# Performance work log

Hardware: AMD Instinct MI355X
Metric: run time of the kernel (lower is better)

The kernel has to match this reference:

```python
import jax, jax.numpy as jnp
import numpy as np

N_NODES = 100000


def gcn_conv(x, src, dst, W, b, n):
    # PyG GCNConv: x' = D^-1/2 (A + I) D^-1/2 (x W) + b
    h = x @ W  # [N, out] transform first (cheaper when out < in)
    loop = jnp.arange(n, dtype=src.dtype)
    s = jnp.concatenate([src, loop])
    d = jnp.concatenate([dst, loop])
    deg = jax.ops.segment_sum(jnp.ones_like(s, dtype=h.dtype), d, num_segments=n)
    dinv = jnp.where(deg > 0, jax.lax.rsqrt(deg), 0.0)
    norm = dinv[s] * dinv[d]  # [E+N]
    msg = h[s] * norm[:, None]  # [E+N, out]
    agg = jax.ops.segment_sum(msg, d, num_segments=n)
    return agg + b


def setup_inputs() -> dict:
    key = jax.random.key(0)
    ks = jax.random.split(key, 12)
    n, E, labels = N_NODES, 1600000, 128
    edges = jax.random.randint(ks[0], (2, E), 0, n, dtype=jnp.int64)
    features = jax.random.normal(ks[1], (n, labels), dtype=jnp.float32)

    def kaiming(k, fan_in, shape):
        return jax.random.normal(k, shape, dtype=jnp.float32) * np.sqrt(2.0 / fan_in)

    return {
        "edges": edges,
        "features": features,
        "W1": kaiming(ks[2], labels, (labels, 64)),
        "b1": jnp.zeros((64,), jnp.float32),
        "W2": kaiming(ks[3], 64, (64, 32)),
        "b2": jnp.zeros((32,), jnp.float32),
        "W3": kaiming(ks[4], 32, (32, 16)),
        "b3": jnp.zeros((16,), jnp.float32),
        "Wfc": kaiming(ks[5], 112, (112, 16)),
        "bfc": jnp.zeros((16,), jnp.float32),
    }


def reference(edges, features, W1, b1, W2, b2, W3, b3, Wfc, bfc):
    n = features.shape[0]
    src, dst = edges[0], edges[1]
    # eval mode: dropout is identity
    f1 = jax.nn.relu(gcn_conv(features, src, dst, W1, b1, n))  # [N, 64]
    f2 = jax.nn.relu(gcn_conv(f1, src, dst, W2, b2, n))        # [N, 32]
    f3 = jax.nn.relu(gcn_conv(f2, src, dst, W3, b3, n))        # [N, 16]
    cat = jnp.concatenate([f1, f2, f3], axis=1)                 # [N, 112]
    return jax.nn.relu(cat @ Wfc + bfc)                         # [N, 16]
```

## Files before the change

### kernel.cpp

```cpp
#include <hip/hip_runtime.h>

typedef unsigned short u16;
typedef float f32x4 __attribute__((ext_vector_type(4)));
typedef short bf16x8 __attribute__((ext_vector_type(8)));

constexpr int SH = 9;
constexpr int NB = 1 << SH;
constexpr int TILE = 4096;

__device__ inline float bf2f(u16 u) {
  union { unsigned int i; float f; } c;
  c.i = ((unsigned int)u) << 16;
  return c.f;
}
__device__ inline u16 f2bf(float f) {
  union { float f; unsigned int i; } c;
  c.f = f;
  unsigned int r = c.i + 0x7fff + ((c.i >> 16) & 1);
  return (u16)(r >> 16);
}

union V8 {
  bf16x8 v;
  short s[8];
  u16 u[8];
};


__global__ void __launch_bounds__(256) k_hist(const int* __restrict__ dst,
                                              int* __restrict__ ghist, int E,
                                              int nblk, int nbk) {
  __shared__ int lcnt[NB];
  int t = threadIdx.x, blk = blockIdx.x;
  for (int i = t; i < nbk; i += 256) lcnt[i] = 0;
  __syncthreads();
  int beg = blk * TILE, end = min(beg + TILE, E);
  for (int e = beg + t; e < end; e += 256) atomicAdd(&lcnt[dst[e] >> SH], 1);
  __syncthreads();
  for (int i = t; i < nbk; i += 256) ghist[i * nblk + blk] = lcnt[i];
}

__global__ void __launch_bounds__(256) k_scanA(int* __restrict__ ghist,
                                               int* __restrict__ bsum, int nblk) {
  __shared__ int sc[256];
  int i = blockIdx.x, t = threadIdx.x;
  int* row = ghist + (size_t)i * nblk;
  int e0 = 2 * t, e1 = 2 * t + 1;
  int a0 = (e0 < nblk) ? row[e0] : 0;
  int a1 = (e1 < nblk) ? row[e1] : 0;
  int s = a0 + a1;
  sc[t] = s;
  __syncthreads();
  for (int o = 1; o < 256; o <<= 1) {
    int x = (t >= o) ? sc[t - o] : 0;
    __syncthreads();
    sc[t] += x;
    __syncthreads();
  }
  int base = sc[t] - s;
  if (e0 < nblk) row[e0] = base;
  if (e1 < nblk) row[e1] = base + a0;
  if (t == 255) bsum[i] = sc[255];
}

__global__ void __launch_bounds__(256) k_part(const int* __restrict__ src,
                                              const int* __restrict__ dst,
                                              const int* __restrict__ goff,
                                              const int* __restrict__ bsum,
                                              int* __restrict__ ebuf, int E,
                                              int nblk, int nbk) {
  __shared__ int lcur[NB];
  __shared__ int sb[256];
  int t = threadIdx.x, blk = blockIdx.x;
  int v = (t < nbk) ? bsum[t] : 0;
  sb[t] = v;
  __syncthreads();
  for (int o = 1; o < 256; o <<= 1) {
    int x = (t >= o) ? sb[t - o] : 0;
    __syncthreads();
    sb[t] += x;
    __syncthreads();
  }
  for (int i = t; i < nbk; i += 256)
    lcur[i] = goff[(size_t)i * nblk + blk] + (i ? sb[i - 1] : 0);
  __syncthreads();
  int beg = blk * TILE, end = min(beg + TILE, E);
  for (int e = beg + t; e < end; e += 256) {
    int s = src[e], d = dst[e];
    int p = atomicAdd(&lcur[d >> SH], 1);
    ebuf[p] = s | ((d & (NB - 1)) << 20);
  }
}

__global__ void __launch_bounds__(256) k_refine(
    const int* __restrict__ ebuf, const int* __restrict__ goff,
    const int* __restrict__ bsum, int* __restrict__ rowptr,
    int* __restrict__ colsrc, float* __restrict__ dinv,
    int n, int nbk, int nblk, int E) {
  __shared__ int cnt[NB];
  __shared__ int cur[NB];
  __shared__ int sc[256];
  __shared__ int bex[256];
  int b = blockIdx.x, t = threadIdx.x;
  {
    int v = (t < nbk) ? bsum[t] : 0;
    bex[t] = v;
    __syncthreads();
    for (int o = 1; o < 256; o <<= 1) {
      int x = (t >= o) ? bex[t - o] : 0;
      __syncthreads();
      bex[t] += x;
      __syncthreads();
    }
  }
  int beg = goff[(size_t)b * nblk] + (b ? bex[b - 1] : 0);
  int end = (b + 1 < nbk) ? goff[(size_t)(b + 1) * nblk] + bex[b] : E;
  cnt[t] = 0;
  cnt[t + 256] = 0;
  __syncthreads();
  for (int i = beg + t; i < end; i += 256) atomicAdd(&cnt[ebuf[i] >> 20], 1);
  __syncthreads();
  int c0 = cnt[2 * t], c1 = cnt[2 * t + 1];
  int a = c0 + c1;
  sc[t] = a;
  __syncthreads();
  for (int o = 1; o < 256; o <<= 1) {
    int x = (t >= o) ? sc[t - o] : 0;
    __syncthreads();
    sc[t] += x;
    __syncthreads();
  }
  int base0 = beg + sc[t] - a;
  int base1 = base0 + c0;
  int node0 = b << SH;
  int n0 = node0 + 2 * t, n1 = n0 + 1;
  cur[2 * t] = base0;
  cur[2 * t + 1] = base1;
  if (n0 <= n) rowptr[n0] = base0;
  if (n1 <= n) rowptr[n1] = base1;
  if (n0 < n) dinv[n0] = rsqrtf((float)(c0 + 1));
  if (n1 < n) dinv[n1] = rsqrtf((float)(c1 + 1));
  if (b == nbk - 1 && t == 0) rowptr[n] = E;
  __syncthreads();
  for (int i = beg + t; i < end; i += 256) {
    int w = ebuf[i];
    int p = atomicAdd(&cur[w >> 20], 1);
    colsrc[p] = w & 0xFFFFF;
  }
}


template <int KC, int FOUT, bool BF16IN>
__global__ void __launch_bounds__(256) k_xform(
    const void* __restrict__ xin, const float* __restrict__ Wg,
    const float* __restrict__ dinv, u16* __restrict__ g, int n) {
  constexpr int FIN = KC * 32;
  constexpr int NC = FOUT / 16;
  constexpr int ASLOTS = 8 * KC * 64;
  constexpr int WSLOTS = KC * NC * 64;
  __shared__ short xa[ASLOTS * 8];
  __shared__ short wb[WSLOTS * 8];

  int t = threadIdx.x;
  int r0 = blockIdx.x * 128;

  for (int s = t; s < WSLOTS; s += 256) {
    int lane = s & 63, q = s >> 6;
    int nc = q % NC, kc = q / NC;
    int col = nc * 16 + (lane & 15);
    int kr = kc * 32 + (lane >> 4) * 8;
    V8 v;
#pragma unroll
    for (int j = 0; j < 8; ++j) v.s[j] = (short)f2bf(Wg[(kr + j) * FOUT + col]);
    *(bf16x8*)&wb[s * 8] = v.v;
  }

  for (int s = t; s < ASLOTS; s += 256) {
    int lane = s & 63, q = s >> 6;
    int kc = q % KC, mtile = q / KC;
    int row = mtile * 16 + (lane & 15);
    int k = kc * 32 + (lane >> 4) * 8;
    int gr = r0 + row;
    V8 v;
    if (gr < n) {
      if constexpr (BF16IN) {
        v.v = *(const bf16x8*)((const u16*)xin + (size_t)gr * FIN + k);
      } else {
        const float* xf = (const float*)xin + (size_t)gr * FIN + k;
        float4 p = *(const float4*)xf;
        float4 q4 = *(const float4*)(xf + 4);
        v.s[0] = (short)f2bf(p.x); v.s[1] = (short)f2bf(p.y);
        v.s[2] = (short)f2bf(p.z); v.s[3] = (short)f2bf(p.w);
        v.s[4] = (short)f2bf(q4.x); v.s[5] = (short)f2bf(q4.y);
        v.s[6] = (short)f2bf(q4.z); v.s[7] = (short)f2bf(q4.w);
      }
    } else {
      for (int j = 0; j < 8; ++j) v.s[j] = 0;
    }
    *(bf16x8*)&xa[s * 8] = v.v;
  }
  __syncthreads();

  int ln = t & 63, wv = t >> 6;
  int m0 = wv * 2;

  bf16x8 bf[KC * NC];
#pragma unroll
  for (int i = 0; i < KC * NC; ++i) bf[i] = *(const bf16x8*)&wb[(i * 64 + ln) * 8];

  f32x4 acc[2][NC];
#pragma unroll
  for (int i = 0; i < 2; ++i)
#pragma unroll
    for (int j = 0; j < NC; ++j) acc[i][j] = {0.f, 0.f, 0.f, 0.f};

#pragma unroll
  for (int kc = 0; kc < KC; ++kc) {
    bf16x8 a0 = *(const bf16x8*)&xa[(((m0 + 0) * KC + kc) * 64 + ln) * 8];
    bf16x8 a1 = *(const bf16x8*)&xa[(((m0 + 1) * KC + kc) * 64 + ln) * 8];
#pragma unroll
    for (int nc = 0; nc < NC; ++nc) {
      acc[0][nc] = __builtin_amdgcn_mfma_f32_16x16x32_bf16(a0, bf[kc * NC + nc], acc[0][nc], 0, 0, 0);
      acc[1][nc] = __builtin_amdgcn_mfma_f32_16x16x32_bf16(a1, bf[kc * NC + nc], acc[1][nc], 0, 0, 0);
    }
  }

  int colb = ln & 15, rq = ln >> 4;
#pragma unroll
  for (int mt2 = 0; mt2 < 2; ++mt2) {
#pragma unroll
    for (int reg = 0; reg < 4; ++reg) {
      int gr = r0 + (m0 + mt2) * 16 + rq * 4 + reg;
      if (gr < n) {
        float di = dinv[gr];
#pragma unroll
        for (int nc = 0; nc < NC; ++nc)
          g[(size_t)gr * FOUT + nc * 16 + colb] = f2bf(acc[mt2][nc][reg] * di);
      }
    }
  }
}


template <int GF, int GOUT, int FCROW0, int FCROWS, int MODE>
__global__ void __launch_bounds__(512) k_gx(
    const u16* __restrict__ gin, const int* __restrict__ rowptr,
    const int* __restrict__ colsrc, const float* __restrict__ dinv,
    const float* __restrict__ bias, const float* __restrict__ Wg,
    const float* __restrict__ Wfc, const float* __restrict__ bfc,
    u16* __restrict__ gout, float* __restrict__ out, int n) {
  constexpr int KC = (GF + 31) / 32;
  constexpr int NCG = (GOUT > 0) ? (GOUT / 16) : 1;
  constexpr int ASLOTS = 8 * KC * 64;
  constexpr int WGSLOTS = (GOUT > 0) ? (KC * NCG * 64) : 64;
  constexpr int WFSLOTS = KC * 64;
  __shared__ short xa[ASLOTS * 8];
  __shared__ short wgb[WGSLOTS * 8];
  __shared__ short wfb[WFSLOTS * 8];

  int t = threadIdx.x;
  int r0 = blockIdx.x * 128;

  {
    V8 z;
#pragma unroll
    for (int j = 0; j < 8; ++j) z.s[j] = 0;
    for (int s = t; s < ASLOTS; s += 512) *(bf16x8*)&xa[s * 8] = z.v;
  }
  if constexpr (GOUT > 0) {
    for (int s = t; s < WGSLOTS; s += 512) {
      int lane = s & 63, q = s >> 6;
      int nc = q % NCG, kc = q / NCG;
      int col = nc * 16 + (lane & 15);
      int kr = kc * 32 + (lane >> 4) * 8;
      V8 v;
#pragma unroll
      for (int j = 0; j < 8; ++j) v.s[j] = (short)f2bf(Wg[(kr + j) * GOUT + col]);
      *(bf16x8*)&wgb[s * 8] = v.v;
    }
  }
  for (int s = t; s < WFSLOTS; s += 512) {
    int lane = s & 63, kc = s >> 6;
    int col = lane & 15;
    int kr = kc * 32 + (lane >> 4) * 8;
    V8 v;
#pragma unroll
    for (int j = 0; j < 8; ++j)
      v.s[j] = (kr + j < FCROWS) ? (short)f2bf(Wfc[(FCROW0 + kr + j) * 16 + col]) : (short)0;
    *(bf16x8*)&wfb[s * 8] = v.v;
  }
  __syncthreads();

  {
    constexpr int LPG = GF / 8;
    constexpr int NPW = 64 / LPG;
    constexpr int PASSES = (128 + NPW * 8 - 1) / (NPW * 8);
    int ln = t & 63, wib = t >> 6;
    int lanein = ln % LPG, grp = ln / LPG;
    int f0 = lanein * 8;
    float bb[8];
#pragma unroll
    for (int j = 0; j < 8; ++j) bb[j] = bias[f0 + j];
#pragma unroll
    for (int pass = 0; pass < PASSES; ++pass) {
      int lr = pass * (NPW * 8) + wib * NPW + grp;
      int gr = r0 + lr;
      if (lr < 128 && gr < n) {
        int b = rowptr[gr], e = rowptr[gr + 1];
        float p0[8], p1[8], p2[8], p3[8];
        {
          V8 u;
          u.v = *(const bf16x8*)&gin[(size_t)gr * GF + f0];
#pragma unroll
          for (int j = 0; j < 8; ++j) {
            p0[j] = bf2f(u.u[j]);
            p1[j] = 0.f; p2[j] = 0.f; p3[j] = 0.f;
          }
        }
        int i = b;
        for (; i + 4 <= e; i += 4) {
          int s0 = colsrc[i + 0], s1 = colsrc[i + 1];
          int s2 = colsrc[i + 2], s3 = colsrc[i + 3];
          V8 u0, u1, u2, u3;
          u0.v = *(const bf16x8*)&gin[(size_t)s0 * GF + f0];
          u1.v = *(const bf16x8*)&gin[(size_t)s1 * GF + f0];
          u2.v = *(const bf16x8*)&gin[(size_t)s2 * GF + f0];
          u3.v = *(const bf16x8*)&gin[(size_t)s3 * GF + f0];
#pragma unroll
          for (int j = 0; j < 8; ++j) {
            p0[j] += bf2f(u0.u[j]);
            p1[j] += bf2f(u1.u[j]);
            p2[j] += bf2f(u2.u[j]);
            p3[j] += bf2f(u3.u[j]);
          }
        }
        for (; i < e; ++i) {
          int s = colsrc[i];
          V8 u;
          u.v = *(const bf16x8*)&gin[(size_t)s * GF + f0];
#pragma unroll
          for (int j = 0; j < 8; ++j) p1[j] += bf2f(u.u[j]);
        }
        float di = dinv[gr];
        V8 o;
#pragma unroll
        for (int j = 0; j < 8; ++j) {
          float a = (p0[j] + p1[j]) + (p2[j] + p3[j]);
          o.u[j] = f2bf(fmaxf(fmaf(a, di, bb[j]), 0.f));
        }
        int kc = f0 >> 5, q = (f0 >> 3) & 3;
        int slot = ((lr >> 4) * KC + kc) * 64 + ((lr & 15) | (q << 4));
        *(bf16x8*)&xa[slot * 8] = o.v;
      }
    }
  }
  __syncthreads();

  int ln = t & 63, wv = t >> 6;
  int m0 = wv;

  bf16x8 wgf[KC * NCG];
  if constexpr (GOUT > 0) {
#pragma unroll
    for (int i = 0; i < KC * NCG; ++i) wgf[i] = *(const bf16x8*)&wgb[(i * 64 + ln) * 8];
  }
  bf16x8 wff[KC];
#pragma unroll
  for (int i = 0; i < KC; ++i) wff[i] = *(const bf16x8*)&wfb[(i * 64 + ln) * 8];

  f32x4 accG[NCG];
  f32x4 accF = {0.f, 0.f, 0.f, 0.f};
#pragma unroll
  for (int j = 0; j < NCG; ++j) accG[j] = {0.f, 0.f, 0.f, 0.f};

#pragma unroll
  for (int kc = 0; kc < KC; ++kc) {
    bf16x8 a0 = *(const bf16x8*)&xa[((m0 * KC + kc) * 64 + ln) * 8];
    if constexpr (GOUT > 0) {
#pragma unroll
      for (int nc = 0; nc < NCG; ++nc)
        accG[nc] = __builtin_amdgcn_mfma_f32_16x16x32_bf16(a0, wgf[kc * NCG + nc], accG[nc], 0, 0, 0);
    }
    accF = __builtin_amdgcn_mfma_f32_16x16x32_bf16(a0, wff[kc], accF, 0, 0, 0);
  }

  int colb = ln & 15, rq = ln >> 4;
#pragma unroll
  for (int reg = 0; reg < 4; ++reg) {
    int gr = r0 + m0 * 16 + rq * 4 + reg;
    if (gr < n) {
      if constexpr (GOUT > 0) {
        float di = dinv[gr];
#pragma unroll
        for (int nc = 0; nc < NCG; ++nc)
          gout[(size_t)gr * GOUT + nc * 16 + colb] = f2bf(accG[nc][reg] * di);
      }
      float fcv = accF[reg];
      size_t oi = (size_t)gr * 16 + colb;
      if constexpr (MODE == 0) {
        out[oi] = fcv;
      } else if constexpr (MODE == 1) {
        out[oi] += fcv;
      } else {
        out[oi] = fmaxf(out[oi] + fcv + bfc[colb], 0.f);
      }
    }
  }
}


extern "C" void kernel_launch(void* const* d_in, const int* in_sizes, int n_in,
                              void* d_out, int out_size, void* d_ws, size_t ws_size,
                              hipStream_t stream) {
  const int* edges = (const int*)d_in[0];
  const float* feat = (const float*)d_in[1];
  const float* W1 = (const float*)d_in[2];
  const float* b1 = (const float*)d_in[3];
  const float* W2 = (const float*)d_in[4];
  const float* b2 = (const float*)d_in[5];
  const float* W3 = (const float*)d_in[6];
  const float* b3 = (const float*)d_in[7];
  const float* Wfc = (const float*)d_in[8];
  const float* bfc = (const float*)d_in[9];
  float* out = (float*)d_out;

  const int E = in_sizes[0] / 2;
  const int n = in_sizes[1] / 128;
  const int* srcp = edges;
  const int* dstp = edges + E;
  const int nbk = (n + NB - 1) >> SH;
  const int nblk = (E + TILE - 1) / TILE;

  char* w = (char*)d_ws;
  auto carve = [&](size_t bytes) {
    void* p = (void*)w;
    w += (bytes + 255) & ~(size_t)255;
    return p;
  };
  int* ghist = (int*)carve((size_t)nbk * nblk * 4);
  int* bsum = (int*)carve(256 * 4);
  int* rowptr = (int*)carve(((size_t)n + 1) * 4);
  float* dinv = (float*)carve((size_t)n * 4);
  int* colsrc = (int*)carve((size_t)E * 4);
  size_t big = (size_t)E * 4 > (size_t)n * 128 ? (size_t)E * 4 : (size_t)n * 128;
  void* shared_big = carve(big);
  int* ebuf = (int*)shared_big;
  u16* g1 = (u16*)shared_big;
  u16* g3 = (u16*)shared_big;
  u16* g2 = (u16*)carve((size_t)n * 32 * 2);

  k_hist<<<nblk, 256, 0, stream>>>(dstp, ghist, E, nblk, nbk);
  k_scanA<<<nbk, 256, 0, stream>>>(ghist, bsum, nblk);
  k_part<<<nblk, 256, 0, stream>>>(srcp, dstp, ghist, bsum, ebuf, E, nblk, nbk);
  k_refine<<<nbk, 256, 0, stream>>>(ebuf, ghist, bsum, rowptr, colsrc, dinv, n, nbk, nblk, E);

  const int xb = (n + 127) / 128;

  k_xform<4, 64, false><<<xb, 256, 0, stream>>>(feat, W1, dinv, g1, n);
  k_gx<64, 32, 0, 64, 0><<<xb, 512, 0, stream>>>(
      g1, rowptr, colsrc, dinv, b1, W2, Wfc, bfc, g2, out, n);
  k_gx<32, 16, 64, 32, 1><<<xb, 512, 0, stream>>>(
      g2, rowptr, colsrc, dinv, b2, W3, Wfc, bfc, g3, out, n);
  k_gx<16, 0, 96, 16, 2><<<xb, 512, 0, stream>>>(
      g3, rowptr, colsrc, dinv, b3, (const float*)nullptr, Wfc, bfc,
      (u16*)nullptr, out, n);
}
```

Measured before the change: 168.0 us.

## Gather directly into MFMA operand registers, dropping the shared-memory staging tile

The fused gather+transform kernel now has each wave own a 16-row tile and gather neighbor features straight into the MFMA A-operand layout in registers. This removes the shared-memory activation buffer, its zeroing, and a block-wide barrier between gather and matmul. Blocks shrink to 256 threads and each wave covers exactly one tile. For the 16-feature layer half the lanes sit idle during the gather, and the wider per-lane accumulators raise register pressure.

```diff
diff --git a/kernel.cpp b/kernel.cpp
--- a/kernel.cpp
+++ b/kernel.cpp
@@ -243,7 +243,7 @@
 
 
 template <int GF, int GOUT, int FCROW0, int FCROWS, int MODE>
-__global__ void __launch_bounds__(512) k_gx(
+__global__ void __launch_bounds__(256) k_gx(
     const u16* __restrict__ gin, const int* __restrict__ rowptr,
     const int* __restrict__ colsrc, const float* __restrict__ dinv,
     const float* __restrict__ bias, const float* __restrict__ Wg,
@@ -251,24 +251,16 @@
     u16* __restrict__ gout, float* __restrict__ out, int n) {
   constexpr int KC = (GF + 31) / 32;
   constexpr int NCG = (GOUT > 0) ? (GOUT / 16) : 1;
-  constexpr int ASLOTS = 8 * KC * 64;
+  constexpr int U = (KC == 2) ? 2 : 4;
   constexpr int WGSLOTS = (GOUT > 0) ? (KC * NCG * 64) : 64;
   constexpr int WFSLOTS = KC * 64;
-  __shared__ short xa[ASLOTS * 8];
   __shared__ short wgb[WGSLOTS * 8];
   __shared__ short wfb[WFSLOTS * 8];
 
   int t = threadIdx.x;
-  int r0 = blockIdx.x * 128;
-
-  {
-    V8 z;
-#pragma unroll
-    for (int j = 0; j < 8; ++j) z.s[j] = 0;
-    for (int s = t; s < ASLOTS; s += 512) *(bf16x8*)&xa[s * 8] = z.v;
-  }
+
   if constexpr (GOUT > 0) {
-    for (int s = t; s < WGSLOTS; s += 512) {
+    for (int s = t; s < WGSLOTS; s += 256) {
       int lane = s & 63, q = s >> 6;
       int nc = q % NCG, kc = q / NCG;
       int col = nc * 16 + (lane & 15);
@@ -279,7 +271,7 @@
       *(bf16x8*)&wgb[s * 8] = v.v;
     }
   }
-  for (int s = t; s < WFSLOTS; s += 512) {
+  for (int s = t; s < WFSLOTS; s += 256) {
     int lane = s & 63, kc = s >> 6;
     int col = lane & 15;
     int kr = kc * 32 + (lane >> 4) * 8;
@@ -291,73 +283,9 @@
   }
   __syncthreads();
 
-  {
-    constexpr int LPG = GF / 8;
-    constexpr int NPW = 64 / LPG;
-    constexpr int PASSES = (128 + NPW * 8 - 1) / (NPW * 8);
-    int ln = t & 63, wib = t >> 6;
-    int lanein = ln % LPG, grp = ln / LPG;
-    int f0 = lanein * 8;
-    float bb[8];
-#pragma unroll
-    for (int j = 0; j < 8; ++j) bb[j] = bias[f0 + j];
-#pragma unroll
-    for (int pass = 0; pass < PASSES; ++pass) {
-      int lr = pass * (NPW * 8) + wib * NPW + grp;
-      int gr = r0 + lr;
-      if (lr < 128 && gr < n) {
-        int b = rowptr[gr], e = rowptr[gr + 1];
-        float p0[8], p1[8], p2[8], p3[8];
-        {
-          V8 u;
-          u.v = *(const bf16x8*)&gin[(size_t)gr * GF + f0];
-#pragma unroll
-          for (int j = 0; j < 8; ++j) {
-            p0[j] = bf2f(u.u[j]);
-            p1[j] = 0.f; p2[j] = 0.f; p3[j] = 0.f;
-          }
-        }
-        int i = b;
-        for (; i + 4 <= e; i += 4) {
-          int s0 = colsrc[i + 0], s1 = colsrc[i + 1];
-          int s2 = colsrc[i + 2], s3 = colsrc[i + 3];
-          V8 u0, u1, u2, u3;
-          u0.v = *(const bf16x8*)&gin[(size_t)s0 * GF + f0];
-          u1.v = *(const bf16x8*)&gin[(size_t)s1 * GF + f0];
-          u2.v = *(const bf16x8*)&gin[(size_t)s2 * GF + f0];
-          u3.v = *(const bf16x8*)&gin[(size_t)s3 * GF + f0];
-#pragma unroll
-          for (int j = 0; j < 8; ++j) {
-            p0[j] += bf2f(u0.u[j]);
-            p1[j] += bf2f(u1.u[j]);
-            p2[j] += bf2f(u2.u[j]);
-            p3[j] += bf2f(u3.u[j]);
-          }
-        }
-        for (; i < e; ++i) {
-          int s = colsrc[i];
-          V8 u;
-          u.v = *(const bf16x8*)&gin[(size_t)s * GF + f0];
-#pragma unroll
-          for (int j = 0; j < 8; ++j) p1[j] += bf2f(u.u[j]);
-        }
-        float di = dinv[gr];
-        V8 o;
-#pragma unroll
-        for (int j = 0; j < 8; ++j) {
-          float a = (p0[j] + p1[j]) + (p2[j] + p3[j]);
-          o.u[j] = f2bf(fmaxf(fmaf(a, di, bb[j]), 0.f));
-        }
-        int kc = f0 >> 5, q = (f0 >> 3) & 3;
-        int slot = ((lr >> 4) * KC + kc) * 64 + ((lr & 15) | (q << 4));
-        *(bf16x8*)&xa[slot * 8] = o.v;
-      }
-    }
-  }
-  __syncthreads();
-
-  int ln = t & 63, wv = t >> 6;
-  int m0 = wv;
+  int ln = t & 63;
+  int r = ln & 15, kq = ln >> 4;
+  const bool vk = (GF > 16) || (kq < 2);
 
   bf16x8 wgf[KC * NCG];
   if constexpr (GOUT > 0) {
@@ -368,41 +296,128 @@
 #pragma unroll
   for (int i = 0; i < KC; ++i) wff[i] = *(const bf16x8*)&wfb[(i * 64 + ln) * 8];
 
-  f32x4 accG[NCG];
-  f32x4 accF = {0.f, 0.f, 0.f, 0.f};
-#pragma unroll
-  for (int j = 0; j < NCG; ++j) accG[j] = {0.f, 0.f, 0.f, 0.f};
-
-#pragma unroll
-  for (int kc = 0; kc < KC; ++kc) {
-    bf16x8 a0 = *(const bf16x8*)&xa[((m0 * KC + kc) * 64 + ln) * 8];
-    if constexpr (GOUT > 0) {
-#pragma unroll
-      for (int nc = 0; nc < NCG; ++nc)
-        accG[nc] = __builtin_amdgcn_mfma_f32_16x16x32_bf16(a0, wgf[kc * NCG + nc], accG[nc], 0, 0, 0);
-    }
-    accF = __builtin_amdgcn_mfma_f32_16x16x32_bf16(a0, wff[kc], accF, 0, 0, 0);
-  }
-
-  int colb = ln & 15, rq = ln >> 4;
-#pragma unroll
-  for (int reg = 0; reg < 4; ++reg) {
-    int gr = r0 + m0 * 16 + rq * 4 + reg;
-    if (gr < n) {
+  float bb[KC][8];
+#pragma unroll
+  for (int c = 0; c < KC; ++c) {
+    if (vk) {
+#pragma unroll
+      for (int j = 0; j < 8; ++j) bb[c][j] = bias[c * 32 + kq * 8 + j];
+    } else {
+#pragma unroll
+      for (int j = 0; j < 8; ++j) bb[c][j] = 0.f;
+    }
+  }
+
+  int wid = blockIdx.x * 4 + (t >> 6);
+  int nw = gridDim.x * 4;
+  int ntiles = (n + 15) / 16;
+
+  for (int tile = wid; tile < ntiles; tile += nw) {
+    int gr = tile * 16 + r;
+    float p[U][KC][8];
+#pragma unroll
+    for (int u = 0; u < U; ++u)
+#pragma unroll
+      for (int c = 0; c < KC; ++c)
+#pragma unroll
+        for (int j = 0; j < 8; ++j) p[u][c][j] = 0.f;
+
+    bool rowok = (gr < n);
+    if (rowok && vk) {
+      int b = rowptr[gr], e = rowptr[gr + 1];
+      {
+        V8 u0;
+#pragma unroll
+        for (int c = 0; c < KC; ++c) {
+          u0.v = *(const bf16x8*)&gin[(size_t)gr * GF + c * 32 + kq * 8];
+#pragma unroll
+          for (int j = 0; j < 8; ++j) p[0][c][j] += bf2f(u0.u[j]);
+        }
+      }
+      int i = b;
+      for (; i + U <= e; i += U) {
+        int sidx[U];
+        V8 ld[U][KC];
+#pragma unroll
+        for (int u = 0; u < U; ++u) sidx[u] = colsrc[i + u];
+#pragma unroll
+        for (int u = 0; u < U; ++u)
+#pragma unroll
+          for (int c = 0; c < KC; ++c)
+            ld[u][c].v = *(const bf16x8*)&gin[(size_t)sidx[u] * GF + c * 32 + kq * 8];
+#pragma unroll
+        for (int u = 0; u < U; ++u)
+#pragma unroll
+          for (int c = 0; c < KC; ++c)
+#pragma unroll
+            for (int j = 0; j < 8; ++j) p[u][c][j] += bf2f(ld[u][c].u[j]);
+      }
+      for (; i < e; ++i) {
+        int s = colsrc[i];
+        V8 u0;
+#pragma unroll
+        for (int c = 0; c < KC; ++c) {
+          u0.v = *(const bf16x8*)&gin[(size_t)s * GF + c * 32 + kq * 8];
+#pragma unroll
+          for (int j = 0; j < 8; ++j) p[U - 1][c][j] += bf2f(u0.u[j]);
+        }
+      }
+    }
+
+    float di = rowok ? dinv[gr] : 0.f;
+    bf16x8 af[KC];
+#pragma unroll
+    for (int c = 0; c < KC; ++c) {
+      V8 o;
+      if (rowok && vk) {
+#pragma unroll
+        for (int j = 0; j < 8; ++j) {
+          float a = p[0][c][j];
+#pragma unroll
+          for (int u = 1; u < U; ++u) a += p[u][c][j];
+          o.u[j] = f2bf(fmaxf(fmaf(a, di, bb[c][j]), 0.f));
+        }
+      } else {
+#pragma unroll
+        for (int j = 0; j < 8; ++j) o.s[j] = 0;
+      }
+      af[c] = o.v;
+    }
+
+    f32x4 accG[NCG];
+    f32x4 accF = {0.f, 0.f, 0.f, 0.f};
+#pragma unroll
+    for (int j = 0; j < NCG; ++j) accG[j] = {0.f, 0.f, 0.f, 0.f};
+#pragma unroll
+    for (int kc = 0; kc < KC; ++kc) {
       if constexpr (GOUT > 0) {
-        float di = dinv[gr];
 #pragma unroll
         for (int nc = 0; nc < NCG; ++nc)
-          gout[(size_t)gr * GOUT + nc * 16 + colb] = f2bf(accG[nc][reg] * di);
-      }
-      float fcv = accF[reg];
-      size_t oi = (size_t)gr * 16 + colb;
-      if constexpr (MODE == 0) {
-        out[oi] = fcv;
-      } else if constexpr (MODE == 1) {
-        out[oi] += fcv;
-      } else {
-        out[oi] = fmaxf(out[oi] + fcv + bfc[colb], 0.f);
+          accG[nc] = __builtin_amdgcn_mfma_f32_16x16x32_bf16(af[kc], wgf[kc * NCG + nc], accG[nc], 0, 0, 0);
+      }
+      accF = __builtin_amdgcn_mfma_f32_16x16x32_bf16(af[kc], wff[kc], accF, 0, 0, 0);
+    }
+
+    int colb = ln & 15, rq = ln >> 4;
+#pragma unroll
+    for (int reg = 0; reg < 4; ++reg) {
+      int g2 = tile * 16 + rq * 4 + reg;
+      if (g2 < n) {
+        if constexpr (GOUT > 0) {
+          float d2 = dinv[g2];
+#pragma unroll
+          for (int nc = 0; nc < NCG; ++nc)
+            gout[(size_t)g2 * GOUT + nc * 16 + colb] = f2bf(accG[nc][reg] * d2);
+        }
+        float fcv = accF[reg];
+        size_t oi = (size_t)g2 * 16 + colb;
+        if constexpr (MODE == 0) {
+          out[oi] = fcv;
+        } else if constexpr (MODE == 1) {
+          out[oi] += fcv;
+        } else {
+          out[oi] = fmaxf(out[oi] + fcv + bfc[colb], 0.f);
+        }
       }
     }
   }
@@ -455,13 +470,15 @@
   k_refine<<<nbk, 256, 0, stream>>>(ebuf, ghist, bsum, rowptr, colsrc, dinv, n, nbk, nblk, E);
 
   const int xb = (n + 127) / 128;
+  const int ntiles = (n + 15) / 16;
+  const int gxb = (ntiles + 3) / 4;
 
   k_xform<4, 64, false><<<xb, 256, 0, stream>>>(feat, W1, dinv, g1, n);
-  k_gx<64, 32, 0, 64, 0><<<xb, 512, 0, stream>>>(
+  k_gx<64, 32, 0, 64, 0><<<gxb, 256, 0, stream>>>(
       g1, rowptr, colsrc, dinv, b1, W2, Wfc, bfc, g2, out, n);
-  k_gx<32, 16, 64, 32, 1><<<xb, 512, 0, stream>>>(
+  k_gx<32, 16, 64, 32, 1><<<gxb, 256, 0, stream>>>(
       g2, rowptr, colsrc, dinv, b2, W3, Wfc, bfc, g3, out, n);
-  k_gx<16, 0, 96, 16, 2><<<xb, 512, 0, stream>>>(
+  k_gx<16, 0, 96, 16, 2><<<gxb, 256, 0, stream>>>(
       g3, rowptr, colsrc, dinv, b3, (const float*)nullptr, Wfc, bfc,
       (u16*)nullptr, out, n);
 }
```

After: 178.1 us. 1.06x slower.
